# Performance work log

Measured on AMD Instinct MI355X. Metric: run time of the kernel, lower is better.

The kernel has to match this reference:

```python
import jax, jax.numpy as jnp
import numpy as np

QS_HIDDEN = 32


def quality_score(feat, W1, b1, W2, b2):
    # (h,5) -> (h,) per-qubit quality in [0,1]
    hdn = jax.nn.relu(feat @ W1 + b1)
    return jax.nn.sigmoid((hdn @ W2 + b2).squeeze(-1))


def _pair_cost(P_log, D, pairs):
    # mean over batch and pairs of sum_{p,q} P_ip * D_pq * P_jq
    Pi = P_log[:, pairs[:, 0], :]  # (batch, E, h)
    Pj = P_log[:, pairs[:, 1], :]  # (batch, E, h)
    return jnp.einsum('beh,hk,bek->be', Pi, D, Pj).mean()


def setup_inputs() -> dict:
    key = jax.random.key(0)
    ks = jax.random.split(key, 10)
    batch, h, L, E = 512, 256, 200, 512
    P = jax.random.uniform(ks[0], (batch, h, h), dtype=jnp.float32)
    P = P / P.sum(-1, keepdims=True)  # row-stochastic (stand-in for doubly stochastic)
    return {
        'P': P,
        'd_error': jax.random.uniform(ks[1], (h, h), dtype=jnp.float32),
        'd_hw': jax.random.uniform(ks[2], (h, h), dtype=jnp.float32),
        'hw_node_features': jax.random.uniform(ks[3], (h, 5), dtype=jnp.float32),
        'qubit_importance': jax.random.uniform(ks[4], (L,), dtype=jnp.float32),
        'W1': jax.random.normal(ks[5], (5, QS_HIDDEN), dtype=jnp.float32) * 0.5,
        'b1': jnp.zeros((QS_HIDDEN,), dtype=jnp.float32),
        'W2': jax.random.normal(ks[6], (QS_HIDDEN, 1), dtype=jnp.float32) * 0.5,
        'b2': jnp.zeros((1,), dtype=jnp.float32),
        'circuit_edge_pairs': jax.random.randint(ks[7], (E, 2), 0, L),
        'cross_circuit_pairs': jax.random.randint(ks[8], (E, 2), 0, L),
        'num_logical': L,
    }


def reference(P, d_error, d_hw, hw_node_features, qubit_importance, W1, b1, W2, b2,
              circuit_edge_pairs, cross_circuit_pairs, num_logical):
    alpha, lambda_sep = 0.3, 0.1
    P_log = P[:, :num_logical, :]  # (batch, L, h)

    # L_surr: error-aware edge loss
    l_surr = _pair_cost(P_log, d_error, circuit_edge_pairs)

    # L_node: node quality loss
    q = quality_score(hw_node_features, W1, b1, W2, b2)  # (h,)
    expected_quality = (P_log * q[None, None, :]).sum(-1)  # (batch, L)
    w_norm = qubit_importance / jnp.clip(qubit_importance.sum(), 1e-8)
    l_node = -(w_norm[None, :] * expected_quality).sum(-1).mean()

    # L_sep: separation loss with max-normalized hardware distance
    d_hw_norm = d_hw / jnp.clip(d_hw.max(), 1e-8)
    l_sep = -_pair_cost(P_log, d_hw_norm, cross_circuit_pairs)

    total = l_surr + alpha * l_node + lambda_sep * l_sep
    return total, l_surr, l_node, l_sep
```

## Files before the change

kernel.cpp:

```cpp
#include <hip/hip_runtime.h>
#include <hip/hip_bf16.h>


typedef __attribute__((ext_vector_type(8))) short short8;
typedef __attribute__((ext_vector_type(4))) float float4_;
typedef __attribute__((ext_vector_type(4))) unsigned int uint4_;
typedef __attribute__((ext_vector_type(2))) unsigned int uint2_;

#define BATCH 512
#define HDIM  256
#define LDIM  200
#define NPAIR 512

#define WS_DCAT_BYTE_OFF 2048

__device__ __forceinline__ unsigned short f2b(float f) {
  unsigned int u = __float_as_uint(f);
  return (unsigned short)((u + 0x7FFFu + ((u >> 16) & 1u)) >> 16);
}
__device__ __forceinline__ float b2f(unsigned short u) {
  return __uint_as_float(((unsigned int)u) << 16);
}

__global__ void s2l_prep(const float* __restrict__ feat, const float* __restrict__ W1,
                         const float* __restrict__ bias1, const float* __restrict__ W2,
                         const float* __restrict__ bias2, const float* __restrict__ qi,
                         const float* __restrict__ d_hw, float* __restrict__ ws) {
  __shared__ float red[8];
  const int tid = threadIdx.x;
  if (tid < 256) {
    float f0 = feat[tid * 5 + 0], f1 = feat[tid * 5 + 1], f2 = feat[tid * 5 + 2];
    float f3 = feat[tid * 5 + 3], f4 = feat[tid * 5 + 4];
    float s = bias2[0];
#pragma unroll
    for (int j = 0; j < 32; ++j) {
      float hd = bias1[j] + f0 * W1[j] + f1 * W1[32 + j] + f2 * W1[64 + j] +
                 f3 * W1[96 + j] + f4 * W1[128 + j];
      hd = fmaxf(hd, 0.f);
      s += hd * W2[j];
    }
    ws[16 + tid] = 1.f / (1.f + expf(-s));
  }
  float v = (tid < LDIM) ? qi[tid] : 0.f;
#pragma unroll
  for (int off = 32; off > 0; off >>= 1) v += __shfl_down(v, off);
  if ((tid & 63) == 0) red[tid >> 6] = v;
  __syncthreads();
  if (tid == 0) ws[3] = 1.f / fmaxf(red[0] + red[1] + red[2] + red[3], 1e-8f);
  float m = 0.f;
  for (int k = tid; k < HDIM * HDIM; k += 256) m = fmaxf(m, d_hw[k]);
#pragma unroll
  for (int off = 32; off > 0; off >>= 1) m = fmaxf(m, __shfl_down(m, off));
  __syncthreads();
  if ((tid & 63) == 0) red[tid >> 6] = m;
  __syncthreads();
  if (tid == 0) {
    float mm = fmaxf(fmaxf(red[0], red[1]), fmaxf(red[2], red[3]));
    ws[4] = 1.f / fmaxf(mm, 1e-8f);
    ws[0] = 0.f; ws[1] = 0.f; ws[2] = 0.f;
  }
}

__global__ void s2l_dcat(const float* __restrict__ d_err, const float* __restrict__ d_hw,
                         const float* __restrict__ ws, unsigned short* __restrict__ DcatT) {
  const int c = blockIdx.x;
  const int h = threadIdx.x;
  float v = (c < 256) ? d_err[h * 256 + c] : d_hw[h * 256 + (c - 256)] * ws[4];
  DcatT[c * 256 + h] = f2b(v);
}

#define P_OFF 0
#define D_OFF 102400
#define T_OFF 135168
#define LDS_BYTES 161792

__global__ __launch_bounds__(512, 2) void s2l_main(
    const float* __restrict__ P, const int* __restrict__ cpairs,
    const int* __restrict__ xpairs, const float* __restrict__ qi,
    float* __restrict__ ws, const unsigned short* __restrict__ DcatT) {
  __shared__ __attribute__((aligned(16))) unsigned char smem[LDS_BYTES];
  const int tid = threadIdx.x;
  const int wave = tid >> 6, lane = tid & 63;
  const int b = blockIdx.x;
  const int nq = wave >> 1;
  const int mg = wave & 1;
  const int ncol = lane & 15;
  const int kg = lane >> 4;

  uint4_ dreg[4];
#pragma unroll
  for (int it = 0; it < 4; ++it) {
    int sg = it * 512 + tid;
    dreg[it] = *(const uint4_*)(DcatT + sg * 8);
  }

  const int s0 = (tid & 31) * 8;
  float qreg[8];
#pragma unroll
  for (int e = 0; e < 8; ++e) qreg[e] = ws[16 + s0 + e];
  const float inv_qs = ws[3];

  const float* Pb = P + (size_t)b * (HDIM * HDIM);
  float lnode = 0.f;
  for (int sg = tid; sg < LDIM * 32; sg += 512) {
    int row = sg >> 5, s = sg & 31;
    float4_ a0 = *(const float4_*)(Pb + row * HDIM + s * 8);
    float4_ a1 = *(const float4_*)(Pb + row * HDIM + s * 8 + 4);
    short8 v;
    v[0] = (short)f2b(a0[0]); v[1] = (short)f2b(a0[1]);
    v[2] = (short)f2b(a0[2]); v[3] = (short)f2b(a0[3]);
    v[4] = (short)f2b(a1[0]); v[5] = (short)f2b(a1[1]);
    v[6] = (short)f2b(a1[2]); v[7] = (short)f2b(a1[3]);
    int swz = (s & 24) | ((s & 7) ^ (row & 7));
    *(short8*)(smem + P_OFF + row * 512 + swz * 16) = v;
    float vq = a0[0] * qreg[0] + a0[1] * qreg[1] + a0[2] * qreg[2] + a0[3] * qreg[3] +
               a1[0] * qreg[4] + a1[1] * qreg[5] + a1[2] * qreg[6] + a1[3] * qreg[7];
    lnode += vq * (qi[row] * inv_qs);
  }
#pragma unroll
  for (int it = 0; it < 4; ++it) {
    int sg = it * 512 + tid, r = sg >> 5, s = sg & 31;
    int swz = (s & 24) | ((s & 7) ^ (r & 7));
    *(uint4_*)(smem + D_OFF + r * 512 + swz * 16) = dreg[it];
  }
  __syncthreads();

  short8 pf[4][8];
#pragma unroll
  for (int nt = 0; nt < 4; ++nt) {
    int tileN = nq * 4 + nt;
    if (tileN < 13) {
      int prow = tileN * 16 + ncol;
#pragma unroll
      for (int ks = 0; ks < 8; ++ks) {
        int slot = ks * 4 + kg;
        int swz = (slot & 24) | ((slot & 7) ^ (prow & 7));
        pf[nt][ks] = *(const short8*)(smem + P_OFF + prow * 512 + swz * 16);
      }
    } else {
      short8 z = {0, 0, 0, 0, 0, 0, 0, 0};
#pragma unroll
      for (int ks = 0; ks < 8; ++ks) pf[nt][ks] = z;
    }
  }

  const int ic = cpairs[2 * tid], jc = cpairs[2 * tid + 1];
  const int ix = xpairs[2 * tid], jx = xpairs[2 * tid + 1];

  float s_surr = 0.f, s_sep = 0.f;
#pragma unroll 1
  for (int ct = 0; ct < 8; ++ct) {
    float4_ acc[4][2];
#pragma unroll
    for (int nt = 0; nt < 4; ++nt)
#pragma unroll
      for (int mt = 0; mt < 2; ++mt) acc[nt][mt] = (float4_){0.f, 0.f, 0.f, 0.f};
#pragma unroll
    for (int ks = 0; ks < 8; ++ks) {
      short8 af[2];
#pragma unroll
      for (int mt = 0; mt < 2; ++mt) {
        int colL = mg * 32 + mt * 16 + ncol;
        int slot = ks * 4 + kg;
        int swz = (slot & 24) | ((slot & 7) ^ (colL & 7));
        af[mt] = *(const short8*)(smem + D_OFF + colL * 512 + swz * 16);
      }
#pragma unroll
      for (int nt = 0; nt < 4; ++nt)
#pragma unroll
        for (int mt = 0; mt < 2; ++mt)
          acc[nt][mt] = __builtin_amdgcn_mfma_f32_16x16x32_bf16(af[mt], pf[nt][ks],
                                                                acc[nt][mt], 0, 0, 0);
    }
#pragma unroll
    for (int nt = 0; nt < 4; ++nt) {
      int tileN = nq * 4 + nt;
      if (tileN >= 13) continue;
      int prow = tileN * 16 + ncol;
#pragma unroll
      for (int mt = 0; mt < 2; ++mt) {
        uint2_ pk;
        pk[0] = (unsigned int)f2b(acc[nt][mt][0]) | ((unsigned int)f2b(acc[nt][mt][1]) << 16);
        pk[1] = (unsigned int)f2b(acc[nt][mt][2]) | ((unsigned int)f2b(acc[nt][mt][3]) << 16);
        int byteInRow = (mg * 32 + mt * 16 + kg * 4) * 2;
        int slot = byteInRow >> 4, off8 = byteInRow & 15;
        *(uint2_*)(smem + T_OFF + prow * 128 + ((slot ^ (prow & 7)) << 4) + off8) = pk;
      }
    }
    __syncthreads();

    uint4_ dnext[4];
    if (ct < 7) {
#pragma unroll
      for (int it = 0; it < 4; ++it) {
        int sg = it * 512 + tid;
        dnext[it] = *(const uint4_*)(DcatT + (size_t)(ct + 1) * 16384 + sg * 8);
      }
    }
    {
      const int i = (ct < 4) ? ic : ix;
      const int j = (ct < 4) ? jc : jx;
      const int pb8 = (ct & 3) * 8;
      float g = 0.f;
#pragma unroll
      for (int s = 0; s < 8; ++s) {
        short8 tv = *(const short8*)(smem + T_OFF + i * 128 + ((s ^ (i & 7)) << 4));
        short8 pv = *(const short8*)(smem + P_OFF + j * 512 + ((pb8 + (s ^ (j & 7))) << 4));
#pragma unroll
        for (int e = 0; e < 8; ++e)
          g += b2f((unsigned short)tv[e]) * b2f((unsigned short)pv[e]);
      }
      if (ct < 4) s_surr += g; else s_sep += g;
    }
    if (ct < 7) {
#pragma unroll
      for (int it = 0; it < 4; ++it) {
        int sg = it * 512 + tid, r = sg >> 5, s = sg & 31;
        int swz = (s & 24) | ((s & 7) ^ (r & 7));
        *(uint4_*)(smem + D_OFF + r * 512 + swz * 16) = dnext[it];
      }
    }
    __syncthreads();
  }

#pragma unroll
  for (int off = 32; off > 0; off >>= 1) {
    s_surr += __shfl_down(s_surr, off);
    s_sep  += __shfl_down(s_sep, off);
    lnode  += __shfl_down(lnode, off);
  }
  float* red = (float*)(smem + D_OFF);
  if (lane == 0) { red[wave * 3] = s_surr; red[wave * 3 + 1] = s_sep; red[wave * 3 + 2] = lnode; }
  __syncthreads();
  if (tid == 0) {
    float a = 0.f, c = 0.f, d = 0.f;
    for (int w = 0; w < 8; ++w) { a += red[w * 3]; c += red[w * 3 + 1]; d += red[w * 3 + 2]; }
    atomicAdd(&ws[0], a);
    atomicAdd(&ws[1], c);
    atomicAdd(&ws[2], d);
  }
}

__global__ void s2l_final(const float* __restrict__ ws, float* __restrict__ out) {
  if (threadIdx.x == 0) {
    const float inv_be = 1.f / (512.f * 512.f);
    float l_surr = ws[0] * inv_be;
    float l_sep = -ws[1] * inv_be;
    float l_node = -ws[2] / 512.f;
    out[0] = l_surr + 0.3f * l_node + 0.1f * l_sep;
    out[1] = l_surr;
    out[2] = l_node;
    out[3] = l_sep;
  }
}

extern "C" void kernel_launch(void* const* d_in, const int* in_sizes, int n_in,
                              void* d_out, int out_size, void* d_ws, size_t ws_size,
                              hipStream_t stream) {
  (void)in_sizes; (void)n_in; (void)out_size; (void)ws_size;
  const float* P     = (const float*)d_in[0];
  const float* d_err = (const float*)d_in[1];
  const float* d_hw  = (const float*)d_in[2];
  const float* feat  = (const float*)d_in[3];
  const float* qi    = (const float*)d_in[4];
  const float* W1    = (const float*)d_in[5];
  const float* bias1 = (const float*)d_in[6];
  const float* W2    = (const float*)d_in[7];
  const float* bias2 = (const float*)d_in[8];
  const int* cpairs  = (const int*)d_in[9];
  const int* xpairs  = (const int*)d_in[10];
  float* ws = (float*)d_ws;
  unsigned short* DcatT = (unsigned short*)((char*)d_ws + WS_DCAT_BYTE_OFF);
  float* out = (float*)d_out;

  s2l_prep<<<dim3(1), dim3(256), 0, stream>>>(feat, W1, bias1, W2, bias2, qi, d_hw, ws);
  s2l_dcat<<<dim3(512), dim3(256), 0, stream>>>(d_err, d_hw, ws, DcatT);
  s2l_main<<<dim3(512), dim3(512), 0, stream>>>(P, cpairs, xpairs, qi, ws, DcatT);
  s2l_final<<<dim3(1), dim3(64), 0, stream>>>(ws, out);
}
```

Measured before the change: 335.6 us.

## Split main kernel per cost half, drop LDS staging of P and D, parallelize prep

The main kernel now runs 1024 blocks, each handling one batch element and one of the two pair costs, instead of one block doing both. P fragments go straight from global memory into MFMA registers, D fragments are read from global or L2 instead of LDS, and the P_j operand of the pair dot product is read in fp32 from global. LDS shrinks to two double-buffered T tiles, allowing four blocks per CU. The d_hw max and the transpose now run as parallel kernels, with a tiled LDS transpose and an atomicMax, rather than one single-block pass. In exchange, P is read from HBM twice per batch element, and the scattered global reads may add latency.

```diff
diff --git a/kernel.cpp b/kernel.cpp
--- a/kernel.cpp
+++ b/kernel.cpp
@@ -1,16 +1,12 @@
 #include <hip/hip_runtime.h>
-#include <hip/hip_bf16.h>
 
 
 typedef __attribute__((ext_vector_type(8))) short short8;
 typedef __attribute__((ext_vector_type(4))) float float4_;
-typedef __attribute__((ext_vector_type(4))) unsigned int uint4_;
 typedef __attribute__((ext_vector_type(2))) unsigned int uint2_;
 
-#define BATCH 512
-#define HDIM  256
-#define LDIM  200
-#define NPAIR 512
+#define HDIM 256
+#define LDIM 200
 
 #define WS_DCAT_BYTE_OFF 2048
 
@@ -21,223 +17,219 @@
 __device__ __forceinline__ float b2f(unsigned short u) {
   return __uint_as_float(((unsigned int)u) << 16);
 }
-
-__global__ void s2l_prep(const float* __restrict__ feat, const float* __restrict__ W1,
-                         const float* __restrict__ bias1, const float* __restrict__ W2,
-                         const float* __restrict__ bias2, const float* __restrict__ qi,
-                         const float* __restrict__ d_hw, float* __restrict__ ws) {
-  __shared__ float red[8];
+__device__ __forceinline__ short8 pack8(float4_ a0, float4_ a1) {
+  short8 f;
+  f[0] = (short)f2b(a0[0]); f[1] = (short)f2b(a0[1]);
+  f[2] = (short)f2b(a0[2]); f[3] = (short)f2b(a0[3]);
+  f[4] = (short)f2b(a1[0]); f[5] = (short)f2b(a1[1]);
+  f[6] = (short)f2b(a1[2]); f[7] = (short)f2b(a1[3]);
+  return f;
+}
+
+__global__ void s2l_scal0(const float* __restrict__ feat, const float* __restrict__ W1,
+                          const float* __restrict__ bias1, const float* __restrict__ W2,
+                          const float* __restrict__ bias2, const float* __restrict__ qi,
+                          float* __restrict__ ws) {
+  __shared__ float red[4];
   const int tid = threadIdx.x;
-  if (tid < 256) {
-    float f0 = feat[tid * 5 + 0], f1 = feat[tid * 5 + 1], f2 = feat[tid * 5 + 2];
-    float f3 = feat[tid * 5 + 3], f4 = feat[tid * 5 + 4];
-    float s = bias2[0];
-#pragma unroll
-    for (int j = 0; j < 32; ++j) {
-      float hd = bias1[j] + f0 * W1[j] + f1 * W1[32 + j] + f2 * W1[64 + j] +
-                 f3 * W1[96 + j] + f4 * W1[128 + j];
-      hd = fmaxf(hd, 0.f);
-      s += hd * W2[j];
-    }
-    ws[16 + tid] = 1.f / (1.f + expf(-s));
-  }
+  float f0 = feat[tid * 5 + 0], f1 = feat[tid * 5 + 1], f2 = feat[tid * 5 + 2];
+  float f3 = feat[tid * 5 + 3], f4 = feat[tid * 5 + 4];
+  float s = bias2[0];
+#pragma unroll
+  for (int j = 0; j < 32; ++j) {
+    float hd = bias1[j] + f0 * W1[j] + f1 * W1[32 + j] + f2 * W1[64 + j] +
+               f3 * W1[96 + j] + f4 * W1[128 + j];
+    s += fmaxf(hd, 0.f) * W2[j];
+  }
+  ws[16 + tid] = 1.f / (1.f + expf(-s));
   float v = (tid < LDIM) ? qi[tid] : 0.f;
 #pragma unroll
   for (int off = 32; off > 0; off >>= 1) v += __shfl_down(v, off);
   if ((tid & 63) == 0) red[tid >> 6] = v;
   __syncthreads();
-  if (tid == 0) ws[3] = 1.f / fmaxf(red[0] + red[1] + red[2] + red[3], 1e-8f);
-  float m = 0.f;
-  for (int k = tid; k < HDIM * HDIM; k += 256) m = fmaxf(m, d_hw[k]);
+  if (tid == 0) {
+    ws[3] = 1.f / fmaxf(red[0] + red[1] + red[2] + red[3], 1e-8f);
+    ws[0] = 0.f; ws[1] = 0.f; ws[2] = 0.f;
+    ((unsigned int*)ws)[5] = 0u;
+  }
+}
+
+__global__ void s2l_dmax(const float* __restrict__ dhw, float* __restrict__ ws) {
+  const int idx = blockIdx.x * 256 + threadIdx.x;
+  float4_ v = *(const float4_*)(dhw + idx * 4);
+  float m = fmaxf(fmaxf(v[0], v[1]), fmaxf(v[2], v[3]));
 #pragma unroll
   for (int off = 32; off > 0; off >>= 1) m = fmaxf(m, __shfl_down(m, off));
+  if ((threadIdx.x & 63) == 0) atomicMax(((unsigned int*)ws) + 5, __float_as_uint(m));
+}
+
+__global__ void s2l_dcat(const float* __restrict__ derr, const float* __restrict__ dhw,
+                         const float* __restrict__ ws, unsigned short* __restrict__ DcatT) {
+  __shared__ float tile[64][65];
+  const int ct = blockIdx.x;
+  const int ht = blockIdx.y;
+  float inv = 1.f;
+  if (ct >= 4) {
+    float mx = __uint_as_float(((const unsigned int*)ws)[5]);
+    inv = 1.f / fmaxf(mx, 1e-8f);
+  }
+  const float* src = (ct < 4) ? derr : dhw;
+  const int c0 = (ct & 3) * 64;
+#pragma unroll
+  for (int k = 0; k < 16; ++k) {
+    int idx = k * 256 + threadIdx.x;
+    int lh = idx >> 6, lc = idx & 63;
+    tile[lh][lc] = src[(ht * 64 + lh) * 256 + c0 + lc] * inv;
+  }
   __syncthreads();
-  if ((tid & 63) == 0) red[tid >> 6] = m;
-  __syncthreads();
-  if (tid == 0) {
-    float mm = fmaxf(fmaxf(red[0], red[1]), fmaxf(red[2], red[3]));
-    ws[4] = 1.f / fmaxf(mm, 1e-8f);
-    ws[0] = 0.f; ws[1] = 0.f; ws[2] = 0.f;
-  }
-}
-
-__global__ void s2l_dcat(const float* __restrict__ d_err, const float* __restrict__ d_hw,
-                         const float* __restrict__ ws, unsigned short* __restrict__ DcatT) {
-  const int c = blockIdx.x;
-  const int h = threadIdx.x;
-  float v = (c < 256) ? d_err[h * 256 + c] : d_hw[h * 256 + (c - 256)] * ws[4];
-  DcatT[c * 256 + h] = f2b(v);
-}
-
-#define P_OFF 0
-#define D_OFF 102400
-#define T_OFF 135168
-#define LDS_BYTES 161792
-
-__global__ __launch_bounds__(512, 2) void s2l_main(
+#pragma unroll
+  for (int k = 0; k < 16; ++k) {
+    int idx = k * 256 + threadIdx.x;
+    int lc = idx >> 6, lh = idx & 63;
+    DcatT[(size_t)(ct * 64 + lc) * HDIM + ht * 64 + lh] = f2b(tile[lh][lc]);
+  }
+}
+
+#define TROWS 208
+#define TSTRIDE 128
+#define TBYTES (TROWS * TSTRIDE)
+#define LDS_BYTES (2 * TBYTES + 64)
+
+__global__ __launch_bounds__(512, 4) void s2l_main(
     const float* __restrict__ P, const int* __restrict__ cpairs,
     const int* __restrict__ xpairs, const float* __restrict__ qi,
     float* __restrict__ ws, const unsigned short* __restrict__ DcatT) {
   __shared__ __attribute__((aligned(16))) unsigned char smem[LDS_BYTES];
   const int tid = threadIdx.x;
   const int wave = tid >> 6, lane = tid & 63;
-  const int b = blockIdx.x;
-  const int nq = wave >> 1;
-  const int mg = wave & 1;
-  const int ncol = lane & 15;
-  const int kg = lane >> 4;
-
-  uint4_ dreg[4];
-#pragma unroll
-  for (int it = 0; it < 4; ++it) {
-    int sg = it * 512 + tid;
-    dreg[it] = *(const uint4_*)(DcatT + sg * 8);
-  }
-
-  const int s0 = (tid & 31) * 8;
-  float qreg[8];
-#pragma unroll
-  for (int e = 0; e < 8; ++e) qreg[e] = ws[16 + s0 + e];
-  const float inv_qs = ws[3];
-
+  const int ncol = lane & 15, kg = lane >> 4;
+  const int half = blockIdx.x >> 9;
+  const int b = blockIdx.x & 511;
   const float* Pb = P + (size_t)b * (HDIM * HDIM);
+  const unsigned short* Dh = DcatT + (size_t)half * 256 * HDIM;
+
+  short8 pf[2][8];
+  const int row0 = wave * 16 + ncol;
+  const int row1 = 128 + wave * 16 + ncol;
+  const bool v1 = (wave < 5);
+  float ln0 = 0.f, ln1 = 0.f;
+  const float* qv = ws + 16;
+#pragma unroll
+  for (int ks = 0; ks < 8; ++ks) {
+    const int h0 = ks * 32 + kg * 8;
+    float4_ a0 = *(const float4_*)(Pb + row0 * HDIM + h0);
+    float4_ a1 = *(const float4_*)(Pb + row0 * HDIM + h0 + 4);
+    pf[0][ks] = pack8(a0, a1);
+    if (half == 0) {
+      float4_ q0 = *(const float4_*)(qv + h0);
+      float4_ q1 = *(const float4_*)(qv + h0 + 4);
+      ln0 += a0[0] * q0[0] + a0[1] * q0[1] + a0[2] * q0[2] + a0[3] * q0[3] +
+             a1[0] * q1[0] + a1[1] * q1[1] + a1[2] * q1[2] + a1[3] * q1[3];
+      if (v1) {
+        float4_ c0 = *(const float4_*)(Pb + row1 * HDIM + h0);
+        float4_ c1 = *(const float4_*)(Pb + row1 * HDIM + h0 + 4);
+        pf[1][ks] = pack8(c0, c1);
+        ln1 += c0[0] * q0[0] + c0[1] * q0[1] + c0[2] * q0[2] + c0[3] * q0[3] +
+               c1[0] * q1[0] + c1[1] * q1[1] + c1[2] * q1[2] + c1[3] * q1[3];
+      } else {
+        pf[1][ks] = (short8){0, 0, 0, 0, 0, 0, 0, 0};
+      }
+    } else {
+      if (v1) {
+        float4_ c0 = *(const float4_*)(Pb + row1 * HDIM + h0);
+        float4_ c1 = *(const float4_*)(Pb + row1 * HDIM + h0 + 4);
+        pf[1][ks] = pack8(c0, c1);
+      } else {
+        pf[1][ks] = (short8){0, 0, 0, 0, 0, 0, 0, 0};
+      }
+    }
+  }
   float lnode = 0.f;
-  for (int sg = tid; sg < LDIM * 32; sg += 512) {
-    int row = sg >> 5, s = sg & 31;
-    float4_ a0 = *(const float4_*)(Pb + row * HDIM + s * 8);
-    float4_ a1 = *(const float4_*)(Pb + row * HDIM + s * 8 + 4);
-    short8 v;
-    v[0] = (short)f2b(a0[0]); v[1] = (short)f2b(a0[1]);
-    v[2] = (short)f2b(a0[2]); v[3] = (short)f2b(a0[3]);
-    v[4] = (short)f2b(a1[0]); v[5] = (short)f2b(a1[1]);
-    v[6] = (short)f2b(a1[2]); v[7] = (short)f2b(a1[3]);
-    int swz = (s & 24) | ((s & 7) ^ (row & 7));
-    *(short8*)(smem + P_OFF + row * 512 + swz * 16) = v;
-    float vq = a0[0] * qreg[0] + a0[1] * qreg[1] + a0[2] * qreg[2] + a0[3] * qreg[3] +
-               a1[0] * qreg[4] + a1[1] * qreg[5] + a1[2] * qreg[6] + a1[3] * qreg[7];
-    lnode += vq * (qi[row] * inv_qs);
-  }
-#pragma unroll
-  for (int it = 0; it < 4; ++it) {
-    int sg = it * 512 + tid, r = sg >> 5, s = sg & 31;
-    int swz = (s & 24) | ((s & 7) ^ (r & 7));
-    *(uint4_*)(smem + D_OFF + r * 512 + swz * 16) = dreg[it];
-  }
-  __syncthreads();
-
-  short8 pf[4][8];
-#pragma unroll
-  for (int nt = 0; nt < 4; ++nt) {
-    int tileN = nq * 4 + nt;
-    if (tileN < 13) {
-      int prow = tileN * 16 + ncol;
-#pragma unroll
-      for (int ks = 0; ks < 8; ++ks) {
-        int slot = ks * 4 + kg;
-        int swz = (slot & 24) | ((slot & 7) ^ (prow & 7));
-        pf[nt][ks] = *(const short8*)(smem + P_OFF + prow * 512 + swz * 16);
-      }
-    } else {
-      short8 z = {0, 0, 0, 0, 0, 0, 0, 0};
-#pragma unroll
-      for (int ks = 0; ks < 8; ++ks) pf[nt][ks] = z;
-    }
-  }
-
-  const int ic = cpairs[2 * tid], jc = cpairs[2 * tid + 1];
-  const int ix = xpairs[2 * tid], jx = xpairs[2 * tid + 1];
-
-  float s_surr = 0.f, s_sep = 0.f;
+  if (half == 0) {
+    const float inv_qs = ws[3];
+    float w0 = qi[row0] * inv_qs;
+    float w1 = (v1 && row1 < LDIM) ? qi[row1] * inv_qs : 0.f;
+    lnode = ln0 * w0 + ln1 * w1;
+  }
+
+  const int* pr = half ? xpairs : cpairs;
+  const int pi = pr[2 * tid], pj = pr[2 * tid + 1];
+  const int piswz = (pi & 7) << 4;
+
+  float gsum = 0.f;
 #pragma unroll 1
-  for (int ct = 0; ct < 8; ++ct) {
-    float4_ acc[4][2];
-#pragma unroll
-    for (int nt = 0; nt < 4; ++nt)
-#pragma unroll
-      for (int mt = 0; mt < 2; ++mt) acc[nt][mt] = (float4_){0.f, 0.f, 0.f, 0.f};
+  for (int ct = 0; ct < 4; ++ct) {
+    unsigned char* Tbuf = smem + (ct & 1) * TBYTES;
+    float4_ acc[2][4];
+#pragma unroll
+    for (int nt = 0; nt < 2; ++nt)
+#pragma unroll
+      for (int mt = 0; mt < 4; ++mt) acc[nt][mt] = (float4_){0.f, 0.f, 0.f, 0.f};
 #pragma unroll
     for (int ks = 0; ks < 8; ++ks) {
-      short8 af[2];
-#pragma unroll
-      for (int mt = 0; mt < 2; ++mt) {
-        int colL = mg * 32 + mt * 16 + ncol;
-        int slot = ks * 4 + kg;
-        int swz = (slot & 24) | ((slot & 7) ^ (colL & 7));
-        af[mt] = *(const short8*)(smem + D_OFF + colL * 512 + swz * 16);
-      }
-#pragma unroll
-      for (int nt = 0; nt < 4; ++nt)
-#pragma unroll
-        for (int mt = 0; mt < 2; ++mt)
-          acc[nt][mt] = __builtin_amdgcn_mfma_f32_16x16x32_bf16(af[mt], pf[nt][ks],
-                                                                acc[nt][mt], 0, 0, 0);
-    }
-#pragma unroll
-    for (int nt = 0; nt < 4; ++nt) {
-      int tileN = nq * 4 + nt;
-      if (tileN >= 13) continue;
-      int prow = tileN * 16 + ncol;
-#pragma unroll
-      for (int mt = 0; mt < 2; ++mt) {
+      short8 af[4];
+#pragma unroll
+      for (int mt = 0; mt < 4; ++mt) {
+        const int c = ct * 64 + mt * 16 + ncol;
+        af[mt] = *(const short8*)(Dh + (size_t)c * HDIM + ks * 32 + kg * 8);
+      }
+#pragma unroll
+      for (int mt = 0; mt < 4; ++mt)
+        acc[0][mt] = __builtin_amdgcn_mfma_f32_16x16x32_bf16(af[mt], pf[0][ks],
+                                                             acc[0][mt], 0, 0, 0);
+      if (v1) {
+#pragma unroll
+        for (int mt = 0; mt < 4; ++mt)
+          acc[1][mt] = __builtin_amdgcn_mfma_f32_16x16x32_bf16(af[mt], pf[1][ks],
+                                                               acc[1][mt], 0, 0, 0);
+      }
+    }
+#pragma unroll
+    for (int nt = 0; nt < 2; ++nt) {
+      if (nt == 1 && !v1) break;
+      const int prow = nt ? row1 : row0;
+#pragma unroll
+      for (int mt = 0; mt < 4; ++mt) {
         uint2_ pk;
         pk[0] = (unsigned int)f2b(acc[nt][mt][0]) | ((unsigned int)f2b(acc[nt][mt][1]) << 16);
         pk[1] = (unsigned int)f2b(acc[nt][mt][2]) | ((unsigned int)f2b(acc[nt][mt][3]) << 16);
-        int byteInRow = (mg * 32 + mt * 16 + kg * 4) * 2;
-        int slot = byteInRow >> 4, off8 = byteInRow & 15;
-        *(uint2_*)(smem + T_OFF + prow * 128 + ((slot ^ (prow & 7)) << 4) + off8) = pk;
+        const int slot = mt * 2 + (kg >> 1), off8 = (kg & 1) * 8;
+        *(uint2_*)(Tbuf + prow * TSTRIDE + ((slot ^ (prow & 7)) << 4) + off8) = pk;
       }
     }
     __syncthreads();
-
-    uint4_ dnext[4];
-    if (ct < 7) {
-#pragma unroll
-      for (int it = 0; it < 4; ++it) {
-        int sg = it * 512 + tid;
-        dnext[it] = *(const uint4_*)(DcatT + (size_t)(ct + 1) * 16384 + sg * 8);
-      }
-    }
     {
-      const int i = (ct < 4) ? ic : ix;
-      const int j = (ct < 4) ? jc : jx;
-      const int pb8 = (ct & 3) * 8;
+      const float* Pj = Pb + pj * HDIM + ct * 64;
+      const unsigned char* Ti = Tbuf + pi * TSTRIDE;
       float g = 0.f;
 #pragma unroll
       for (int s = 0; s < 8; ++s) {
-        short8 tv = *(const short8*)(smem + T_OFF + i * 128 + ((s ^ (i & 7)) << 4));
-        short8 pv = *(const short8*)(smem + P_OFF + j * 512 + ((pb8 + (s ^ (j & 7))) << 4));
-#pragma unroll
-        for (int e = 0; e < 8; ++e)
-          g += b2f((unsigned short)tv[e]) * b2f((unsigned short)pv[e]);
-      }
-      if (ct < 4) s_surr += g; else s_sep += g;
-    }
-    if (ct < 7) {
-#pragma unroll
-      for (int it = 0; it < 4; ++it) {
-        int sg = it * 512 + tid, r = sg >> 5, s = sg & 31;
-        int swz = (s & 24) | ((s & 7) ^ (r & 7));
-        *(uint4_*)(smem + D_OFF + r * 512 + swz * 16) = dnext[it];
-      }
-    }
-    __syncthreads();
+        short8 tv = *(const short8*)(Ti + (((s << 4)) ^ piswz));
+        float4_ p0 = *(const float4_*)(Pj + s * 8);
+        float4_ p1 = *(const float4_*)(Pj + s * 8 + 4);
+#pragma unroll
+        for (int e = 0; e < 4; ++e) {
+          g += b2f((unsigned short)tv[e]) * p0[e];
+          g += b2f((unsigned short)tv[e + 4]) * p1[e];
+        }
+      }
+      gsum += g;
+    }
   }
 
 #pragma unroll
   for (int off = 32; off > 0; off >>= 1) {
-    s_surr += __shfl_down(s_surr, off);
-    s_sep  += __shfl_down(s_sep, off);
-    lnode  += __shfl_down(lnode, off);
-  }
-  float* red = (float*)(smem + D_OFF);
-  if (lane == 0) { red[wave * 3] = s_surr; red[wave * 3 + 1] = s_sep; red[wave * 3 + 2] = lnode; }
+    gsum += __shfl_down(gsum, off);
+    lnode += __shfl_down(lnode, off);
+  }
+  float* red = (float*)(smem + 2 * TBYTES);
+  if (lane == 0) { red[wave * 2] = gsum; red[wave * 2 + 1] = lnode; }
   __syncthreads();
   if (tid == 0) {
-    float a = 0.f, c = 0.f, d = 0.f;
-    for (int w = 0; w < 8; ++w) { a += red[w * 3]; c += red[w * 3 + 1]; d += red[w * 3 + 2]; }
-    atomicAdd(&ws[0], a);
-    atomicAdd(&ws[1], c);
-    atomicAdd(&ws[2], d);
+    float g = 0.f, l = 0.f;
+    for (int w = 0; w < 8; ++w) { g += red[2 * w]; l += red[2 * w + 1]; }
+    atomicAdd(&ws[half], g);
+    if (half == 0) atomicAdd(&ws[2], l);
   }
 }
 
@@ -273,8 +265,9 @@
   unsigned short* DcatT = (unsigned short*)((char*)d_ws + WS_DCAT_BYTE_OFF);
   float* out = (float*)d_out;
 
-  s2l_prep<<<dim3(1), dim3(256), 0, stream>>>(feat, W1, bias1, W2, bias2, qi, d_hw, ws);
-  s2l_dcat<<<dim3(512), dim3(256), 0, stream>>>(d_err, d_hw, ws, DcatT);
-  s2l_main<<<dim3(512), dim3(512), 0, stream>>>(P, cpairs, xpairs, qi, ws, DcatT);
+  s2l_scal0<<<dim3(1), dim3(256), 0, stream>>>(feat, W1, bias1, W2, bias2, qi, ws);
+  s2l_dmax<<<dim3(64), dim3(256), 0, stream>>>(d_hw, ws);
+  s2l_dcat<<<dim3(8, 4), dim3(256), 0, stream>>>(d_err, d_hw, ws, DcatT);
+  s2l_main<<<dim3(1024), dim3(512), 0, stream>>>(P, cpairs, xpairs, qi, ws, DcatT);
   s2l_final<<<dim3(1), dim3(64), 0, stream>>>(ws, out);
 }
```

Result: slower. 399.4 us (+19.0%).

## Parallelize prep and transpose, read D from global, double-buffer T, use fdot2

Applied to the files above, without the earlier changes.

The d_hw max reduction is spread across 64 blocks with atomicMax, and a memset clears the workspace first. The D transpose now goes through a tiled shared-memory kernel. The main kernel drops the LDS staging of D and loads MFMA A-fragments straight from global/L2. The intermediate T buffer is double-buffered so one barrier per column tile is removed, and the pair dot products are spread over 8 lanes each using bf16 fdot2. These aim to cut the serial prep time and LDS sync overhead, at the cost of more global loads inside the MFMA loop. The reduction epilogue also gains some leftover dead code and per-wave atomics for lnode.

```diff
diff --git a/kernel.cpp b/kernel.cpp
--- a/kernel.cpp
+++ b/kernel.cpp
@@ -1,16 +1,13 @@
 #include <hip/hip_runtime.h>
-#include <hip/hip_bf16.h>
 
 
 typedef __attribute__((ext_vector_type(8))) short short8;
 typedef __attribute__((ext_vector_type(4))) float float4_;
+typedef __attribute__((ext_vector_type(2))) unsigned int uint2_;
 typedef __attribute__((ext_vector_type(4))) unsigned int uint4_;
-typedef __attribute__((ext_vector_type(2))) unsigned int uint2_;
-
-#define BATCH 512
-#define HDIM  256
-#define LDIM  200
-#define NPAIR 512
+
+#define HDIM 256
+#define LDIM 200
 
 #define WS_DCAT_BYTE_OFF 2048
 
@@ -22,13 +19,44 @@
   return __uint_as_float(((unsigned int)u) << 16);
 }
 
+#if defined(__has_builtin)
+#if __has_builtin(__builtin_amdgcn_fdot2_f32_bf16)
+#define HAVE_FDOT2 1
+#endif
+#endif
+#ifdef HAVE_FDOT2
+typedef __attribute__((ext_vector_type(2))) __bf16 bf16x2;
+#endif
+
+__device__ __forceinline__ float dot8acc(uint4_ a, uint4_ b, float acc) {
+#ifdef HAVE_FDOT2
+#pragma unroll
+  for (int d = 0; d < 4; ++d) {
+    union { unsigned int u; bf16x2 v; } ua, ub;
+    ua.u = a[d]; ub.u = b[d];
+    acc = __builtin_amdgcn_fdot2_f32_bf16(ua.v, ub.v, acc, false);
+  }
+#else
+#pragma unroll
+  for (int d = 0; d < 4; ++d) {
+    float alo = __uint_as_float(a[d] << 16);
+    float ahi = __uint_as_float(a[d] & 0xffff0000u);
+    float blo = __uint_as_float(b[d] << 16);
+    float bhi = __uint_as_float(b[d] & 0xffff0000u);
+    acc = fmaf(alo, blo, acc);
+    acc = fmaf(ahi, bhi, acc);
+  }
+#endif
+  return acc;
+}
+
 __global__ void s2l_prep(const float* __restrict__ feat, const float* __restrict__ W1,
                          const float* __restrict__ bias1, const float* __restrict__ W2,
                          const float* __restrict__ bias2, const float* __restrict__ qi,
-                         const float* __restrict__ d_hw, float* __restrict__ ws) {
-  __shared__ float red[8];
+                         const float* __restrict__ dhw, float* __restrict__ ws) {
   const int tid = threadIdx.x;
-  if (tid < 256) {
+  if (blockIdx.x == 0) {
+    __shared__ float red[4];
     float f0 = feat[tid * 5 + 0], f1 = feat[tid * 5 + 1], f2 = feat[tid * 5 + 2];
     float f3 = feat[tid * 5 + 3], f4 = feat[tid * 5 + 4];
     float s = bias2[0];
@@ -36,43 +64,58 @@
     for (int j = 0; j < 32; ++j) {
       float hd = bias1[j] + f0 * W1[j] + f1 * W1[32 + j] + f2 * W1[64 + j] +
                  f3 * W1[96 + j] + f4 * W1[128 + j];
-      hd = fmaxf(hd, 0.f);
-      s += hd * W2[j];
+      s += fmaxf(hd, 0.f) * W2[j];
     }
     ws[16 + tid] = 1.f / (1.f + expf(-s));
-  }
-  float v = (tid < LDIM) ? qi[tid] : 0.f;
-#pragma unroll
-  for (int off = 32; off > 0; off >>= 1) v += __shfl_down(v, off);
-  if ((tid & 63) == 0) red[tid >> 6] = v;
-  __syncthreads();
-  if (tid == 0) ws[3] = 1.f / fmaxf(red[0] + red[1] + red[2] + red[3], 1e-8f);
-  float m = 0.f;
-  for (int k = tid; k < HDIM * HDIM; k += 256) m = fmaxf(m, d_hw[k]);
-#pragma unroll
-  for (int off = 32; off > 0; off >>= 1) m = fmaxf(m, __shfl_down(m, off));
-  __syncthreads();
-  if ((tid & 63) == 0) red[tid >> 6] = m;
-  __syncthreads();
-  if (tid == 0) {
-    float mm = fmaxf(fmaxf(red[0], red[1]), fmaxf(red[2], red[3]));
-    ws[4] = 1.f / fmaxf(mm, 1e-8f);
-    ws[0] = 0.f; ws[1] = 0.f; ws[2] = 0.f;
-  }
-}
-
-__global__ void s2l_dcat(const float* __restrict__ d_err, const float* __restrict__ d_hw,
+    float v = (tid < LDIM) ? qi[tid] : 0.f;
+#pragma unroll
+    for (int off = 32; off > 0; off >>= 1) v += __shfl_down(v, off);
+    if ((tid & 63) == 0) red[tid >> 6] = v;
+    __syncthreads();
+    if (tid == 0) ws[3] = 1.f / fmaxf(red[0] + red[1] + red[2] + red[3], 1e-8f);
+  } else {
+    const int idx = (blockIdx.x - 1) * 1024 + tid * 4;
+    float4_ v = *(const float4_*)(dhw + idx);
+    float m = fmaxf(fmaxf(v[0], v[1]), fmaxf(v[2], v[3]));
+#pragma unroll
+    for (int off = 32; off > 0; off >>= 1) m = fmaxf(m, __shfl_down(m, off));
+    if ((tid & 63) == 0) atomicMax(((unsigned int*)ws) + 5, __float_as_uint(m));
+  }
+}
+
+__global__ void s2l_dcat(const float* __restrict__ derr, const float* __restrict__ dhw,
                          const float* __restrict__ ws, unsigned short* __restrict__ DcatT) {
-  const int c = blockIdx.x;
-  const int h = threadIdx.x;
-  float v = (c < 256) ? d_err[h * 256 + c] : d_hw[h * 256 + (c - 256)] * ws[4];
-  DcatT[c * 256 + h] = f2b(v);
+  __shared__ float tile[64][65];
+  const int ct = blockIdx.x;
+  const int ht = blockIdx.y;
+  float inv = 1.f;
+  if (ct >= 4) {
+    float mx = __uint_as_float(((const unsigned int*)ws)[5]);
+    inv = 1.f / fmaxf(mx, 1e-8f);
+  }
+  const float* src = (ct < 4) ? derr : dhw;
+  const int c0 = (ct & 3) * 64;
+#pragma unroll
+  for (int k = 0; k < 16; ++k) {
+    int idx = k * 256 + threadIdx.x;
+    int lh = idx >> 6, lc = idx & 63;
+    tile[lh][lc] = src[(ht * 64 + lh) * 256 + c0 + lc] * inv;
+  }
+  __syncthreads();
+#pragma unroll
+  for (int k = 0; k < 16; ++k) {
+    int idx = k * 256 + threadIdx.x;
+    int lc = idx >> 6, lh = idx & 63;
+    DcatT[(size_t)(ct * 64 + lc) * HDIM + ht * 64 + lh] = f2b(tile[lh][lc]);
+  }
 }
 
 #define P_OFF 0
-#define D_OFF 102400
-#define T_OFF 135168
-#define LDS_BYTES 161792
+#define T_OFF 102400
+#define TSTRIDE 128
+#define TBYTES (208 * TSTRIDE)
+#define RED_OFF (T_OFF + 2 * TBYTES)
+#define LDS_BYTES (RED_OFF + 64)
 
 __global__ __launch_bounds__(512, 2) void s2l_main(
     const float* __restrict__ P, const int* __restrict__ cpairs,
@@ -86,13 +129,6 @@
   const int mg = wave & 1;
   const int ncol = lane & 15;
   const int kg = lane >> 4;
-
-  uint4_ dreg[4];
-#pragma unroll
-  for (int it = 0; it < 4; ++it) {
-    int sg = it * 512 + tid;
-    dreg[it] = *(const uint4_*)(DcatT + sg * 8);
-  }
 
   const int s0 = (tid & 31) * 8;
   float qreg[8];
@@ -117,39 +153,39 @@
                a1[0] * qreg[4] + a1[1] * qreg[5] + a1[2] * qreg[6] + a1[3] * qreg[7];
     lnode += vq * (qi[row] * inv_qs);
   }
-#pragma unroll
-  for (int it = 0; it < 4; ++it) {
-    int sg = it * 512 + tid, r = sg >> 5, s = sg & 31;
-    int swz = (s & 24) | ((s & 7) ^ (r & 7));
-    *(uint4_*)(smem + D_OFF + r * 512 + swz * 16) = dreg[it];
+  if (tid < 256) {
+    int row = 200 + (tid >> 5), s = tid & 31;
+    int swz = (s & 24) | ((s & 7) ^ (row & 7));
+    *(short8*)(smem + P_OFF + row * 512 + swz * 16) = (short8){0, 0, 0, 0, 0, 0, 0, 0};
   }
   __syncthreads();
 
   short8 pf[4][8];
 #pragma unroll
   for (int nt = 0; nt < 4; ++nt) {
-    int tileN = nq * 4 + nt;
-    if (tileN < 13) {
-      int prow = tileN * 16 + ncol;
-#pragma unroll
-      for (int ks = 0; ks < 8; ++ks) {
-        int slot = ks * 4 + kg;
-        int swz = (slot & 24) | ((slot & 7) ^ (prow & 7));
-        pf[nt][ks] = *(const short8*)(smem + P_OFF + prow * 512 + swz * 16);
-      }
-    } else {
-      short8 z = {0, 0, 0, 0, 0, 0, 0, 0};
-#pragma unroll
-      for (int ks = 0; ks < 8; ++ks) pf[nt][ks] = z;
-    }
-  }
-
-  const int ic = cpairs[2 * tid], jc = cpairs[2 * tid + 1];
-  const int ix = xpairs[2 * tid], jx = xpairs[2 * tid + 1];
-
+    int prow = (nq * 4 + nt) * 16 + ncol;
+#pragma unroll
+    for (int ks = 0; ks < 8; ++ks) {
+      int slot = ks * 4 + kg;
+      int swz = (slot & 24) | ((slot & 7) ^ (prow & 7));
+      pf[nt][ks] = *(const short8*)(smem + P_OFF + prow * 512 + swz * 16);
+    }
+  }
+
+  const int so = tid & 7, p0 = tid >> 3;
+  int ip[8], jp[8];
   float s_surr = 0.f, s_sep = 0.f;
+
 #pragma unroll 1
   for (int ct = 0; ct < 8; ++ct) {
+    if ((ct & 3) == 0) {
+      const int* pr = (ct < 4) ? cpairs : xpairs;
+#pragma unroll
+      for (int k = 0; k < 8; ++k) {
+        int2 pp = *(const int2*)(pr + 2 * (p0 + 64 * k));
+        ip[k] = pp.x; jp[k] = pp.y;
+      }
+    }
     float4_ acc[4][2];
 #pragma unroll
     for (int nt = 0; nt < 4; ++nt)
@@ -160,10 +196,8 @@
       short8 af[2];
 #pragma unroll
       for (int mt = 0; mt < 2; ++mt) {
-        int colL = mg * 32 + mt * 16 + ncol;
-        int slot = ks * 4 + kg;
-        int swz = (slot & 24) | ((slot & 7) ^ (colL & 7));
-        af[mt] = *(const short8*)(smem + D_OFF + colL * 512 + swz * 16);
+        int c = ct * 64 + mg * 32 + mt * 16 + ncol;
+        af[mt] = *(const short8*)(DcatT + c * HDIM + ks * 32 + kg * 8);
       }
 #pragma unroll
       for (int nt = 0; nt < 4; ++nt)
@@ -172,55 +206,32 @@
           acc[nt][mt] = __builtin_amdgcn_mfma_f32_16x16x32_bf16(af[mt], pf[nt][ks],
                                                                 acc[nt][mt], 0, 0, 0);
     }
+    unsigned char* Tbuf = smem + T_OFF + (ct & 1) * TBYTES;
 #pragma unroll
     for (int nt = 0; nt < 4; ++nt) {
-      int tileN = nq * 4 + nt;
-      if (tileN >= 13) continue;
-      int prow = tileN * 16 + ncol;
+      int prow = (nq * 4 + nt) * 16 + ncol;
 #pragma unroll
       for (int mt = 0; mt < 2; ++mt) {
         uint2_ pk;
         pk[0] = (unsigned int)f2b(acc[nt][mt][0]) | ((unsigned int)f2b(acc[nt][mt][1]) << 16);
         pk[1] = (unsigned int)f2b(acc[nt][mt][2]) | ((unsigned int)f2b(acc[nt][mt][3]) << 16);
-        int byteInRow = (mg * 32 + mt * 16 + kg * 4) * 2;
-        int slot = byteInRow >> 4, off8 = byteInRow & 15;
-        *(uint2_*)(smem + T_OFF + prow * 128 + ((slot ^ (prow & 7)) << 4) + off8) = pk;
+        int slot = (mg * 32 + mt * 16 + kg * 4) >> 3;
+        int off8 = (kg & 1) * 8;
+        *(uint2_*)(Tbuf + prow * TSTRIDE + ((slot ^ (prow & 7)) << 4) + off8) = pk;
       }
     }
     __syncthreads();
 
-    uint4_ dnext[4];
-    if (ct < 7) {
-#pragma unroll
-      for (int it = 0; it < 4; ++it) {
-        int sg = it * 512 + tid;
-        dnext[it] = *(const uint4_*)(DcatT + (size_t)(ct + 1) * 16384 + sg * 8);
-      }
-    }
-    {
-      const int i = (ct < 4) ? ic : ix;
-      const int j = (ct < 4) ? jc : jx;
-      const int pb8 = (ct & 3) * 8;
-      float g = 0.f;
-#pragma unroll
-      for (int s = 0; s < 8; ++s) {
-        short8 tv = *(const short8*)(smem + T_OFF + i * 128 + ((s ^ (i & 7)) << 4));
-        short8 pv = *(const short8*)(smem + P_OFF + j * 512 + ((pb8 + (s ^ (j & 7))) << 4));
-#pragma unroll
-        for (int e = 0; e < 8; ++e)
-          g += b2f((unsigned short)tv[e]) * b2f((unsigned short)pv[e]);
-      }
-      if (ct < 4) s_surr += g; else s_sep += g;
-    }
-    if (ct < 7) {
-#pragma unroll
-      for (int it = 0; it < 4; ++it) {
-        int sg = it * 512 + tid, r = sg >> 5, s = sg & 31;
-        int swz = (s & 24) | ((s & 7) ^ (r & 7));
-        *(uint4_*)(smem + D_OFF + r * 512 + swz * 16) = dnext[it];
-      }
-    }
-    __syncthreads();
+    float g = 0.f;
+#pragma unroll
+    for (int k = 0; k < 8; ++k) {
+      const int i = ip[k], j = jp[k];
+      uint4_ tv = *(const uint4_*)(Tbuf + i * TSTRIDE + ((so ^ (i & 7)) << 4));
+      int q = ((ct & 3) * 8) | (so ^ (j & 7));
+      uint4_ pv = *(const uint4_*)(smem + P_OFF + j * 512 + (q << 4));
+      g = dot8acc(tv, pv, g);
+    }
+    if (ct < 4) s_surr += g; else s_sep += g;
   }
 
 #pragma unroll
@@ -229,16 +240,22 @@
     s_sep  += __shfl_down(s_sep, off);
     lnode  += __shfl_down(lnode, off);
   }
-  float* red = (float*)(smem + D_OFF);
-  if (lane == 0) { red[wave * 3] = s_surr; red[wave * 3 + 1] = s_sep; red[wave * 3 + 2] = lnode; }
+  float* red = (float*)(smem + RED_OFF);
+  if (lane == 0) { red[wave] = s_surr; red[8 + wave] = s_sep; }
+  __syncthreads();
+  if (lane == 0 && wave == 0) {
+  }
+  __syncthreads();
+  if (lane == 0) ((float*)(smem + RED_OFF))[0] = red[0];
+  if (lane == 0) red[8 + 8 + wave] = lnode;
   __syncthreads();
   if (tid == 0) {
-    float a = 0.f, c = 0.f, d = 0.f;
-    for (int w = 0; w < 8; ++w) { a += red[w * 3]; c += red[w * 3 + 1]; d += red[w * 3 + 2]; }
+    float a = 0.f, c = 0.f;
+    for (int w = 0; w < 8; ++w) { a += red[w]; c += red[8 + w]; }
     atomicAdd(&ws[0], a);
     atomicAdd(&ws[1], c);
-    atomicAdd(&ws[2], d);
-  }
+  }
+  if (lane == 0) atomicAdd(&ws[2], lnode);
 }
 
 __global__ void s2l_final(const float* __restrict__ ws, float* __restrict__ out) {
@@ -273,8 +290,9 @@
   unsigned short* DcatT = (unsigned short*)((char*)d_ws + WS_DCAT_BYTE_OFF);
   float* out = (float*)d_out;
 
-  s2l_prep<<<dim3(1), dim3(256), 0, stream>>>(feat, W1, bias1, W2, bias2, qi, d_hw, ws);
-  s2l_dcat<<<dim3(512), dim3(256), 0, stream>>>(d_err, d_hw, ws, DcatT);
+  hipMemsetAsync(d_ws, 0, 64, stream);
+  s2l_prep<<<dim3(65), dim3(256), 0, stream>>>(feat, W1, bias1, W2, bias2, qi, d_hw, ws);
+  s2l_dcat<<<dim3(8, 4), dim3(256), 0, stream>>>(d_err, d_hw, ws, DcatT);
   s2l_main<<<dim3(512), dim3(512), 0, stream>>>(P, cpairs, xpairs, qi, ws, DcatT);
   s2l_final<<<dim3(1), dim3(64), 0, stream>>>(ws, out);
 }
```

Result: no change. 339.2 us (+1.1%).
